# Optimization experiments

Measured on AMD Instinct MI355X. Metric: run time of the kernel, lower is better.

## Reference

```python
import jax, jax.numpy as jnp
import numpy as np
import math

M = 0.65
S = 64.0
WEIGHT = 0.003
COS_M = math.cos(M)
SIN_M = math.sin(M)
THRESHOLD = math.cos(math.pi - M)
MM = math.sin(math.pi - M) * M

B, D, C = 512, 512, 100000


def l2_norm(x, axis):
    return x / jnp.linalg.norm(x, ord=2, axis=axis, keepdims=True)


def setup_inputs() -> dict:
    key = jax.random.key(0)
    k1, k2, k3 = jax.random.split(key, 3)
    embbedings = jax.random.normal(k1, (B, D), dtype=jnp.float32)
    kernel = 0.01 * jax.random.normal(k2, (D, C), dtype=jnp.float32)  # Parameter init std=0.01
    t = jnp.zeros((1,), dtype=jnp.float32)  # running buffer
    label = jax.random.randint(k3, (B,), 0, C, dtype=jnp.int64)
    return {"embbedings": embbedings, "kernel": kernel, "t": t, "label": label}


def reference(embbedings, kernel, t, label):
    emb = l2_norm(embbedings, axis=1)          # [B, D]
    kernel_norm = l2_norm(kernel, axis=0)      # [D, C]
    cos_theta = jnp.clip(emb @ kernel_norm, -1.0, 1.0)  # [B, C]
    origin_cos = jax.lax.stop_gradient(cos_theta)       # torch: clone under no_grad

    rows = jnp.arange(cos_theta.shape[0])
    target_logit = cos_theta[rows, label][:, None]       # [B, 1]
    sin_theta = jnp.sqrt(1.0 - target_logit ** 2)
    cos_theta_m = target_logit * COS_M - sin_theta * SIN_M

    mask = cos_theta > cos_theta_m                       # [B, C]
    final_target_logit = jnp.where(target_logit > THRESHOLD,
                                   cos_theta_m, target_logit - MM)

    # buffer update (no_grad), used immediately for hard-example reweighting
    t_new = jax.lax.stop_gradient(target_logit.mean()) * 0.01 + 0.99 * t  # [1]

    ct = jnp.where(mask, cos_theta * (t_new + cos_theta), cos_theta)
    ct = ct.at[rows, label].set(final_target_logit[:, 0])  # scatter_ on dim 1
    output = ct * S  # dropout with p=0 is identity

    # angular center loss; center is detached (no_grad clone) in torch
    center = jax.lax.stop_gradient(kernel.T)[label]       # [B, D]
    c_norm = l2_norm(center, axis=1)
    cos_theta_center = jnp.clip(jnp.sum(emb * c_norm, axis=1), -1.0, 1.0)
    center_loss = jnp.mean(jnp.arccos(cos_theta_center) ** 1.5)

    return output, origin_cos * S, S * WEIGHT * center_loss
```

## Files before the change

### kernel.cpp

```cpp
#include <hip/hip_runtime.h>
#include <hip/hip_bf16.h>
#include <stdint.h>

#define B_M 512
#define D_K 512
#define C_N 100000
#define S_SCALE 64.0f
#define W_LOSS 0.003f
#define COS_M_C 0.79608379854905604f
#define SIN_M_C 0.60518640573603957f
#define THRESH_C (-0.79608379854905604f)
#define MM_C 0.39337116372842573f

typedef __bf16 bf16x8 __attribute__((ext_vector_type(8)));
typedef float f32x4 __attribute__((ext_vector_type(4)));

typedef const __attribute__((address_space(1))) unsigned char* gptr_t;
typedef __attribute__((address_space(3))) unsigned char* sptr_t;

__device__ __forceinline__ unsigned short f2bf(float f) {
  __bf16 h = (__bf16)f;
  return __builtin_bit_cast(unsigned short, h);
}

__global__ __launch_bounds__(256) void prep_kernel(
    const float* __restrict__ emb, const float* __restrict__ Kg,
    const int* __restrict__ label, unsigned char* __restrict__ wsA,
    float* __restrict__ tl)
{
  int b = blockIdx.x, t = threadIdx.x;
  __shared__ float row[512];
  __shared__ float r1[256], r2[256];

  float2 v = ((const float2*)(emb + (size_t)b * 512))[t];
  r1[t] = v.x * v.x + v.y * v.y;
  __syncthreads();
  for (int s = 128; s > 0; s >>= 1) {
    if (t < s) r1[t] += r1[t + s];
    __syncthreads();
  }
  float inv = 1.0f / sqrtf(r1[0]);
  float e0 = v.x * inv, e1 = v.y * inv;
  row[2 * t] = e0;
  row[2 * t + 1] = e1;

  {
    int mhalf = b >> 8, lrow = b & 255;
    int kk = t >> 5;
    int byte_in = (4 * (t & 31)) ^ ((lrow & 7) << 4);
    ushort2 h;
    h.x = f2bf(e0);
    h.y = f2bf(e1);
    *(ushort2*)(wsA + (size_t)(mhalf * 8 + kk) * 32768 + lrow * 128 + byte_in) = h;
  }
  __syncthreads();

  int lab = label[b];
  const float* kc = Kg + lab;
  float dot = 0.f, csq = 0.f;
  for (int d = t; d < 512; d += 256) {
    float kv = kc[(size_t)d * C_N];
    dot += row[d] * kv;
    csq += kv * kv;
  }
  r1[t] = dot;
  r2[t] = csq;
  __syncthreads();
  for (int s = 128; s > 0; s >>= 1) {
    if (t < s) { r1[t] += r1[t + s]; r2[t] += r2[t + s]; }
    __syncthreads();
  }
  if (t == 0) {
    float tlv = r1[0] / sqrtf(r2[0]);
    tl[b] = fminf(1.f, fmaxf(-1.f, tlv));
  }
}

__global__ __launch_bounds__(512) void finalize_kernel(
    const float* __restrict__ tl, const float* __restrict__ t_in,
    float* __restrict__ ctm, float* __restrict__ ftl,
    float* __restrict__ tnew, float* __restrict__ out3)
{
  int t = threadIdx.x;
  float v = tl[t];
  __shared__ float r1[512], r2[512];
  float ac = acosf(v);
  r1[t] = v;
  r2[t] = ac * sqrtf(ac);
  __syncthreads();
  for (int s = 256; s > 0; s >>= 1) {
    if (t < s) { r1[t] += r1[t + s]; r2[t] += r2[t + s]; }
    __syncthreads();
  }
  if (t == 0) {
    tnew[0] = 0.99f * t_in[0] + 0.01f * (r1[0] / 512.0f);
    out3[0] = S_SCALE * W_LOSS * (r2[0] / 512.0f);
  }
  float st = sqrtf(fmaxf(0.f, 1.f - v * v));
  float cm = v * COS_M_C - st * SIN_M_C;
  ctm[t] = cm;
  ftl[t] = (v > THRESH_C) ? cm : (v - MM_C);
}

#define LDS_TOTAL 81920

__global__ __launch_bounds__(512, 2) void gemm_kernel(
    const float* __restrict__ Kg, const unsigned char* __restrict__ wsA,
    const float* __restrict__ ctm_g, const float* __restrict__ ftl_g,
    const int* __restrict__ label, const float* __restrict__ tnew_g,
    float* __restrict__ out1, float* __restrict__ out2)
{
  __shared__ __align__(16) unsigned char smem[LDS_TOTAL];

  int t = threadIdx.x;
  int lane = t & 63, wv = t >> 6;
  int wm = wv >> 2, wn = wv & 3;

  int bid = blockIdx.x;
  {
    const int q8 = 1564 / 8, r8 = 1564 % 8;
    int xcd = bid & 7, seq = bid >> 3;
    bid = (xcd < r8 ? xcd * (q8 + 1) : r8 * (q8 + 1) + (xcd - r8) * q8) + seq;
  }
  int pid = bid >> 1, mhalf = bid & 1;
  long c0 = (long)pid * 128;

  int c = t & 127, kseg = t >> 7;
  bool binb = (c0 + c) < C_N;
  const float* Bcol = Kg + c0 + c;

  f32x4 acc[8][2] = {};
  float csq = 0.f;
  float bf[16];

  const unsigned char* wsTile = wsA + (size_t)mhalf * (8 * 32768);
  unsigned char* smemB = smem + 65536;

  {
#pragma unroll
    for (int i = 0; i < 4; ++i) {
      int off = wv * 4096 + i * 1024;
      __builtin_amdgcn_global_load_lds((gptr_t)(wsTile + off + lane * 16),
                                       (sptr_t)(smem + off), 16, 0, 0);
    }
#pragma unroll
    for (int i = 0; i < 16; ++i) bf[i] = binb ? Bcol[(size_t)(kseg * 16 + i) * C_N] : 0.f;
#pragma unroll
    for (int i = 0; i < 16; ++i) csq += bf[i] * bf[i];
    union { unsigned short u[16]; uint4 q[2]; } pk;
#pragma unroll
    for (int i = 0; i < 16; ++i) pk.u[i] = f2bf(bf[i]);
    unsigned char* brow = smemB + c * 128;
#pragma unroll
    for (int h = 0; h < 2; ++h)
      *(uint4*)(brow + ((kseg * 32 + h * 16) ^ ((c & 7) << 4))) = pk.q[h];
    asm volatile("s_waitcnt vmcnt(0)" ::: "memory");
    __builtin_amdgcn_sched_barrier(0);
    __syncthreads();
  }

  for (int kkt = 0; kkt < 8; ++kkt) {
    int cur = kkt & 1;
    if (kkt < 7) {
      const unsigned char* tA = wsTile + (size_t)(kkt + 1) * 32768;
#pragma unroll
      for (int i = 0; i < 4; ++i) {
        int off = wv * 4096 + i * 1024;
        __builtin_amdgcn_global_load_lds((gptr_t)(tA + off + lane * 16),
                                         (sptr_t)(smem + (cur ^ 1) * 32768 + off), 16, 0, 0);
      }
      int kbase = (kkt + 1) * 64 + kseg * 16;
#pragma unroll
      for (int i = 0; i < 16; ++i) bf[i] = binb ? Bcol[(size_t)(kbase + i) * C_N] : 0.f;
    }

    const unsigned char* Ab = smem + cur * 32768;
#pragma unroll
    for (int ks = 0; ks < 2; ++ks) {
      int kb = ks * 64 + (lane >> 4) * 16;
      bf16x8 bfr[2];
#pragma unroll
      for (int nf = 0; nf < 2; ++nf) {
        int n = wn * 32 + nf * 16 + (lane & 15);
        bfr[nf] = *(const bf16x8*)(smemB + n * 128 + (kb ^ ((n & 7) << 4)));
      }
#pragma unroll
      for (int mf = 0; mf < 8; ++mf) {
        int m = wm * 128 + mf * 16 + (lane & 15);
        bf16x8 afr = *(const bf16x8*)(Ab + m * 128 + (kb ^ ((m & 7) << 4)));
        acc[mf][0] = __builtin_amdgcn_mfma_f32_16x16x32_bf16(afr, bfr[0], acc[mf][0], 0, 0, 0);
        acc[mf][1] = __builtin_amdgcn_mfma_f32_16x16x32_bf16(afr, bfr[1], acc[mf][1], 0, 0, 0);
      }
    }

    asm volatile("s_waitcnt vmcnt(0)" ::: "memory");
    __builtin_amdgcn_sched_barrier(0);
    __syncthreads();

    if (kkt < 7) {
#pragma unroll
      for (int i = 0; i < 16; ++i) csq += bf[i] * bf[i];
      union { unsigned short u[16]; uint4 q[2]; } pk;
#pragma unroll
      for (int i = 0; i < 16; ++i) pk.u[i] = f2bf(bf[i]);
      unsigned char* brow = smemB + c * 128;
#pragma unroll
      for (int h = 0; h < 2; ++h)
        *(uint4*)(brow + ((kseg * 32 + h * 16) ^ ((c & 7) << 4))) = pk.q[h];
    }
    __syncthreads();
  }

  float* colpart = (float*)(smemB);
  float* invn    = (float*)(smemB + 2048);
  float* ctm_s   = (float*)(smemB + 2560);
  float* ftl_s   = (float*)(smemB + 3584);
  int*   lab_s   = (int*)  (smemB + 4608);
  colpart[t] = csq;
  if (t < 256) {
    ctm_s[t] = ctm_g[mhalf * 256 + t];
    ftl_s[t] = ftl_g[mhalf * 256 + t];
    lab_s[t] = label[mhalf * 256 + t];
  }
  __syncthreads();
  if (t < 128) {
    float s = colpart[t] + colpart[128 + t] + colpart[256 + t] + colpart[384 + t];
    invn[t] = 1.0f / sqrtf(fmaxf(s, 1e-30f));
  }
  __syncthreads();
  float tn = tnew_g[0];

  for (int q = 0; q < 2; ++q) {
    if (wm == q) {
#pragma unroll
      for (int mf = 0; mf < 8; ++mf) {
#pragma unroll
        for (int nf = 0; nf < 2; ++nf) {
#pragma unroll
          for (int j = 0; j < 4; ++j) {
            int row = mf * 16 + (lane >> 4) * 4 + j;
            int col = wn * 32 + nf * 16 + (lane & 15);
            *(float*)(smem + row * 512 + ((col * 4) ^ (((row >> 2) & 3) << 6))) =
                acc[mf][nf][j];
          }
        }
      }
    }
    __syncthreads();
#pragma unroll
    for (int rr = 0; rr < 8; ++rr) {
      int row = rr * 16 + (t >> 5);
      int cb = (t & 31) * 4;
      f32x4 v = *(const f32x4*)(smem + row * 512 + ((cb * 4) ^ (((row >> 2) & 3) << 6)));
      long cgs = c0 + cb;
      if (cgs < C_N) {
        int lrow = q * 128 + row;
        float cm = ctm_s[lrow], fl = ftl_s[lrow];
        int lb = lab_s[lrow];
        f32x4 iv = *(const f32x4*)(invn + cb);
        f32x4 o1v, o2v;
#pragma unroll
        for (int jj = 0; jj < 4; ++jj) {
          float cosv = fminf(1.f, fmaxf(-1.f, v[jj] * iv[jj]));
          o2v[jj] = cosv * S_SCALE;
          float ct = (cosv > cm) ? cosv * (tn + cosv) : cosv;
          if (lb == (int)(cgs + jj)) ct = fl;
          o1v[jj] = ct * S_SCALE;
        }
        size_t idx = (size_t)(mhalf * 256 + lrow) * C_N + cgs;
        *(f32x4*)(out1 + idx) = o1v;
        *(f32x4*)(out2 + idx) = o2v;
      }
    }
    __syncthreads();
  }
}

extern "C" void kernel_launch(void* const* d_in, const int* in_sizes, int n_in,
                              void* d_out, int out_size, void* d_ws, size_t ws_size,
                              hipStream_t stream)
{
  const float* emb   = (const float*)d_in[0];
  const float* Kg    = (const float*)d_in[1];
  const float* t_in  = (const float*)d_in[2];
  const int*   label = (const int*)d_in[3];

  float* out1 = (float*)d_out;
  float* out2 = out1 + (size_t)B_M * C_N;
  float* out3 = out1 + 2 * (size_t)B_M * C_N;

  unsigned char* wsA = (unsigned char*)d_ws;
  float* tl   = (float*)((unsigned char*)d_ws + 524288);
  float* ctm  = tl + 512;
  float* ftl  = ctm + 512;
  float* tnew = ftl + 512;

  prep_kernel<<<512, 256, 0, stream>>>(emb, Kg, label, wsA, tl);
  finalize_kernel<<<1, 512, 0, stream>>>(tl, t_in, ctm, ftl, tnew, out3);
  int nb = 2 * ((C_N + 127) / 128);
  gemm_kernel<<<nb, 512, 0, stream>>>(Kg, wsA, ctm, ftl, label, tnew, out1, out2);
}
```

Before: 170.0 us.

## Double-buffer kernel-column register prefetch two tiles ahead and use nontemporal output stores

Prefetches the fp32 kernel-column slices two K-tiles ahead into alternating register buffers, using partial vmcnt waits so global loads overlap more than one MFMA stage. The loop is fully unrolled and one barrier per iteration is dropped. Output stores become nontemporal to avoid polluting cache with the large streamed outputs. Costs extra registers (a second 16-float buffer), which may reduce occupancy, and the vmcnt(16) counting depends on the compiler's exact instruction ordering.

```diff
diff --git a/kernel.cpp b/kernel.cpp
--- a/kernel.cpp
+++ b/kernel.cpp
@@ -127,14 +127,31 @@
 
   int c = t & 127, kseg = t >> 7;
   bool binb = (c0 + c) < C_N;
-  const float* Bcol = Kg + c0 + c;
+  const float* Bcol = Kg + c0 + c + (size_t)kseg * 16 * C_N;
 
   f32x4 acc[8][2] = {};
   float csq = 0.f;
-  float bf[16];
+  float bf0[16], bf1[16];
 
   const unsigned char* wsTile = wsA + (size_t)mhalf * (8 * 32768);
   unsigned char* smemB = smem + 65536;
+  unsigned char* browB = smemB + c * 128;
+
+#define LOAD_B(dst, j)                                                       \
+  {                                                                          \
+    const float* src = Bcol + (size_t)((j) * 64) * C_N;                      \
+    _Pragma("unroll") for (int i = 0; i < 16; ++i)                           \
+        dst[i] = binb ? src[(size_t)i * C_N] : 0.f;                          \
+  }
+
+#define WRITE_B(src)                                                         \
+  {                                                                          \
+    _Pragma("unroll") for (int i = 0; i < 16; ++i) csq += src[i] * src[i];   \
+    union { unsigned short u[16]; uint4 q[2]; } pk;                          \
+    _Pragma("unroll") for (int i = 0; i < 16; ++i) pk.u[i] = f2bf(src[i]);   \
+    _Pragma("unroll") for (int h = 0; h < 2; ++h)                            \
+      *(uint4*)(browB + ((kseg * 32 + h * 16) ^ ((c & 7) << 4))) = pk.q[h];  \
+  }
 
   {
 #pragma unroll
@@ -143,22 +160,18 @@
       __builtin_amdgcn_global_load_lds((gptr_t)(wsTile + off + lane * 16),
                                        (sptr_t)(smem + off), 16, 0, 0);
     }
-#pragma unroll
-    for (int i = 0; i < 16; ++i) bf[i] = binb ? Bcol[(size_t)(kseg * 16 + i) * C_N] : 0.f;
-#pragma unroll
-    for (int i = 0; i < 16; ++i) csq += bf[i] * bf[i];
-    union { unsigned short u[16]; uint4 q[2]; } pk;
-#pragma unroll
-    for (int i = 0; i < 16; ++i) pk.u[i] = f2bf(bf[i]);
-    unsigned char* brow = smemB + c * 128;
-#pragma unroll
-    for (int h = 0; h < 2; ++h)
-      *(uint4*)(brow + ((kseg * 32 + h * 16) ^ ((c & 7) << 4))) = pk.q[h];
-    asm volatile("s_waitcnt vmcnt(0)" ::: "memory");
-    __builtin_amdgcn_sched_barrier(0);
-    __syncthreads();
-  }
-
+    __builtin_amdgcn_sched_barrier(0);
+    LOAD_B(bf0, 0);
+    __builtin_amdgcn_sched_barrier(0);
+    LOAD_B(bf1, 1);
+    __builtin_amdgcn_sched_barrier(0);
+    asm volatile("s_waitcnt vmcnt(16)" ::: "memory");
+    __builtin_amdgcn_sched_barrier(0);
+    WRITE_B(bf0);
+    __syncthreads();
+  }
+
+#pragma unroll
   for (int kkt = 0; kkt < 8; ++kkt) {
     int cur = kkt & 1;
     if (kkt < 7) {
@@ -169,9 +182,11 @@
         __builtin_amdgcn_global_load_lds((gptr_t)(tA + off + lane * 16),
                                          (sptr_t)(smem + (cur ^ 1) * 32768 + off), 16, 0, 0);
       }
-      int kbase = (kkt + 1) * 64 + kseg * 16;
-#pragma unroll
-      for (int i = 0; i < 16; ++i) bf[i] = binb ? Bcol[(size_t)(kbase + i) * C_N] : 0.f;
+      __builtin_amdgcn_sched_barrier(0);
+    }
+    if (kkt < 6) {
+      if (kkt & 1) { LOAD_B(bf1, kkt + 2); } else { LOAD_B(bf0, kkt + 2); }
+      __builtin_amdgcn_sched_barrier(0);
     }
 
     const unsigned char* Ab = smem + cur * 32768;
@@ -193,22 +208,18 @@
       }
     }
 
-    asm volatile("s_waitcnt vmcnt(0)" ::: "memory");
+    if (kkt < 6) {
+      asm volatile("s_waitcnt vmcnt(16)" ::: "memory");
+    } else {
+      asm volatile("s_waitcnt vmcnt(0)" ::: "memory");
+    }
     __builtin_amdgcn_sched_barrier(0);
     __syncthreads();
 
     if (kkt < 7) {
-#pragma unroll
-      for (int i = 0; i < 16; ++i) csq += bf[i] * bf[i];
-      union { unsigned short u[16]; uint4 q[2]; } pk;
-#pragma unroll
-      for (int i = 0; i < 16; ++i) pk.u[i] = f2bf(bf[i]);
-      unsigned char* brow = smemB + c * 128;
-#pragma unroll
-      for (int h = 0; h < 2; ++h)
-        *(uint4*)(brow + ((kseg * 32 + h * 16) ^ ((c & 7) << 4))) = pk.q[h];
-    }
-    __syncthreads();
+      if (kkt & 1) { WRITE_B(bf0); } else { WRITE_B(bf1); }
+      __syncthreads();
+    }
   }
 
   float* colpart = (float*)(smemB);
@@ -268,12 +279,14 @@
           o1v[jj] = ct * S_SCALE;
         }
         size_t idx = (size_t)(mhalf * 256 + lrow) * C_N + cgs;
-        *(f32x4*)(out1 + idx) = o1v;
-        *(f32x4*)(out2 + idx) = o2v;
-      }
-    }
-    __syncthreads();
-  }
+        __builtin_nontemporal_store(o1v, (f32x4*)(out1 + idx));
+        __builtin_nontemporal_store(o2v, (f32x4*)(out2 + idx));
+      }
+    }
+    __syncthreads();
+  }
+#undef LOAD_B
+#undef WRITE_B
 }
 
 extern "C" void kernel_launch(void* const* d_in, const int* in_sizes, int n_in,
```

Measured after the change: 159.2 us. 1.07x faster.
